# Kernel optimization log

Hardware: AMD Instinct MI355X
Metric: run time of the kernel (lower is better)

## Reference

```python
import jax, jax.numpy as jnp
import numpy as np

N = 50000      # nodes
E = 800000     # edges (before self-loops)
IN = 64        # in_channels
HID = 128      # hidden
HEADS = 4
C = HID // HEADS  # per-head dim = 32
EPS_BN = 1e-5


def setup_inputs() -> dict:
    key = jax.random.key(0)
    ks = jax.random.split(key, 40)
    f32 = jnp.float32
    def rn(i, shape, s=0.05):
        return jax.random.normal(ks[i], shape, f32) * s
    def un(i, shape, lo=0.5, hi=1.5):
        return jax.random.uniform(ks[i], shape, f32, lo, hi)
    inp = {
        'x': jax.random.normal(ks[0], (N, IN), f32),
        'edge_index': jax.random.randint(ks[1], (2, E), 0, N, jnp.int64),
        # pre: Linear(IN, HID) + BatchNorm1d(HID)
        'W_pre': rn(2, (IN, HID)), 'b_pre': rn(3, (HID,)),
        'g_pre': un(4, (HID,)), 'be_pre': rn(5, (HID,)),
        'm_pre': rn(6, (HID,), 0.1), 'v_pre': un(7, (HID,)),
        # gat1 (GATv2Conv): lin_l, lin_r, att, bias
        'Wl1': rn(8, (HID, HID)), 'bl1': rn(9, (HID,)),
        'Wr1': rn(10, (HID, HID)), 'br1': rn(11, (HID,)),
        'att1': rn(12, (HEADS, C)), 'bias1': rn(13, (HID,)),
        'g1': un(14, (HID,)), 'be1': rn(15, (HID,)),
        'm1': rn(16, (HID,), 0.1), 'v1': un(17, (HID,)),
        # gat2
        'Wl2': rn(18, (HID, HID)), 'bl2': rn(19, (HID,)),
        'Wr2': rn(20, (HID, HID)), 'br2': rn(21, (HID,)),
        'att2': rn(22, (HEADS, C)), 'bias2': rn(23, (HID,)),
        'g2': un(24, (HID,)), 'be2': rn(25, (HID,)),
        'm2': rn(26, (HID,), 0.1), 'v2': un(27, (HID,)),
        # out head: Linear(HID, HID//2) -> LeakyReLU -> Linear(HID//2, 1)
        'Wo1': rn(28, (HID, HID // 2)), 'bo1': rn(29, (HID // 2,)),
        'Wo2': rn(30, (HID // 2, 1)), 'bo2': rn(31, (1,)),
    }
    return inp


def _bn(x, g, b, m, v):
    # eval-mode BatchNorm1d with running stats
    return (x - m) * jax.lax.rsqrt(v + EPS_BN) * g + b


def _gatv2(x, src, dst, Wl, bl, Wr, br, att, bias):
    # PyG GATv2Conv, concat=True, negative_slope=0.2, eval (no dropout)
    n = x.shape[0]
    xl = (x @ Wl + bl).reshape(n, HEADS, C)   # messages from source
    xr = (x @ Wr + br).reshape(n, HEADS, C)   # target side
    xj = xl[src]                              # [E2, H, C] gather
    s = jax.nn.leaky_relu(xr[dst] + xj, 0.2)
    logits = jnp.einsum('ehc,hc->eh', s, att)  # [E2, H]
    # segment softmax over destination nodes
    mx = jax.ops.segment_max(logits, dst, num_segments=n)
    e = jnp.exp(logits - mx[dst])
    den = jax.ops.segment_sum(e, dst, num_segments=n)
    alpha = e / (den[dst] + 1e-16)
    out = jax.ops.segment_sum(xj * alpha[:, :, None], dst, num_segments=n)
    return out.reshape(n, HID) + bias


def reference(x, edge_index,
              W_pre, b_pre, g_pre, be_pre, m_pre, v_pre,
              Wl1, bl1, Wr1, br1, att1, bias1, g1, be1, m1, v1,
              Wl2, bl2, Wr2, br2, att2, bias2, g2, be2, m2, v2,
              Wo1, bo1, Wo2, bo2):
    n = x.shape[0]
    # add self loops (PyG GATv2Conv default add_self_loops=True)
    loop = jnp.arange(n, dtype=edge_index.dtype)
    src = jnp.concatenate([edge_index[0], loop])
    dst = jnp.concatenate([edge_index[1], loop])

    x = jax.nn.leaky_relu(_bn(x @ W_pre + b_pre, g_pre, be_pre, m_pre, v_pre), 0.1)
    h = x
    x = _gatv2(x, src, dst, Wl1, bl1, Wr1, br1, att1, bias1)
    x = jax.nn.leaky_relu(_bn(x, g1, be1, m1, v1), 0.1) + h
    h = x
    x = _gatv2(x, src, dst, Wl2, bl2, Wr2, br2, att2, bias2)
    x = jax.nn.leaky_relu(_bn(x, g2, be2, m2, v2), 0.1) + h
    x = jax.nn.leaky_relu(x @ Wo1 + bo1, 0.1)
    return x @ Wo2 + bo2
```

## Files before the change

kernel.cpp:

```cpp
#include <hip/hip_runtime.h>
#include <hip/hip_bf16.h>
#include <hip/hip_fp16.h>

#define NN 50000
#define EE 800000
#define SCAN_B 196

typedef unsigned int uint;
typedef unsigned short ushort;
typedef __attribute__((ext_vector_type(8))) short s16x8;
typedef __attribute__((ext_vector_type(4))) float f32x4;
typedef __attribute__((ext_vector_type(2))) _Float16 h16x2;

__device__ __forceinline__ float lrelu(float x, float s){ return fmaxf(x, x * s); }

__device__ __forceinline__ ushort bf16_rne(float x){
  uint u = __float_as_uint(x);
  return (ushort)((u + 0x7FFFu + ((u >> 16) & 1u)) >> 16);
}
__device__ __forceinline__ float bf16f(ushort h){ return __uint_as_float(((uint)h) << 16); }

__device__ __forceinline__ float dpp_add4(float x){
  int v = __float_as_int(x), t;
  t = __builtin_amdgcn_update_dpp(0, v, 0xB1, 0xF, 0xF, true);
  v = __float_as_int(__int_as_float(v) + __int_as_float(t));
  t = __builtin_amdgcn_update_dpp(0, v, 0x4E, 0xF, 0xF, true);
  v = __float_as_int(__int_as_float(v) + __int_as_float(t));
  return __int_as_float(v);
}

__device__ __forceinline__ float dpp_add16(float x){
  int v = __float_as_int(x), t;
  t = __builtin_amdgcn_update_dpp(0, v, 0xB1, 0xF, 0xF, true);
  v = __float_as_int(__int_as_float(v) + __int_as_float(t));
  t = __builtin_amdgcn_update_dpp(0, v, 0x4E, 0xF, 0xF, true);
  v = __float_as_int(__int_as_float(v) + __int_as_float(t));
  t = __builtin_amdgcn_update_dpp(0, v, 0x141, 0xF, 0xF, true);
  v = __float_as_int(__int_as_float(v) + __int_as_float(t));
  t = __builtin_amdgcn_update_dpp(0, v, 0x140, 0xF, 0xF, true);
  v = __float_as_int(__int_as_float(v) + __int_as_float(t));
  return __int_as_float(v);
}


__global__ void detect_kernel(const int* __restrict__ ei, int* __restrict__ flag){
  __shared__ int any;
  if (threadIdx.x == 0) any = 0;
  __syncthreads();
  if (ei[2 * threadIdx.x + 1] != 0) atomicOr(&any, 1);
  __syncthreads();
  if (threadIdx.x == 0) *flag = (any == 0) ? 1 : 0;
}

__global__ void zero1_kernel(int* __restrict__ a, int n){
  int i = blockIdx.x * blockDim.x + threadIdx.x;
  if (i < n) a[i] = 0;
}

__global__ void count_kernel(const int* __restrict__ ei, const int* __restrict__ flag,
                             int* __restrict__ deg){
  int e = blockIdx.x * blockDim.x + threadIdx.x;
  if (e >= EE) return;
  int d;
  if (*flag){
    const long long* eil = (const long long*)ei;
    d = (int)eil[EE + e];
  } else {
    d = ei[EE + e];
  }
  atomicAdd(&deg[d], 1);
}

__global__ void scan1_kernel(const int* __restrict__ deg, int* __restrict__ rowptr,
                             int* __restrict__ bsum){
  __shared__ int tmp[256];
  int tid = threadIdx.x;
  int idx = blockIdx.x * 256 + tid;
  int v = (idx < NN) ? deg[idx] : 0;
  tmp[tid] = v;
  __syncthreads();
  for (int off = 1; off < 256; off <<= 1){
    int t = (tid >= off) ? tmp[tid - off] : 0;
    __syncthreads();
    tmp[tid] += t;
    __syncthreads();
  }
  if (idx < NN) rowptr[idx] = tmp[tid] - v;
  if (tid == 255) bsum[blockIdx.x] = tmp[255];
}

__global__ void scan2_kernel(const int* __restrict__ bsum, int* __restrict__ boff,
                             int* __restrict__ rowptr){
  __shared__ int tmp[256];
  int tid = threadIdx.x;
  int v = (tid < SCAN_B) ? bsum[tid] : 0;
  tmp[tid] = v;
  __syncthreads();
  for (int off = 1; off < 256; off <<= 1){
    int t = (tid >= off) ? tmp[tid - off] : 0;
    __syncthreads();
    tmp[tid] += t;
    __syncthreads();
  }
  if (tid < SCAN_B) boff[tid] = tmp[tid] - v;
  if (tid == 255) rowptr[NN] = tmp[255];
}

__global__ void scan3_kernel(int* __restrict__ rowptr, const int* __restrict__ boff,
                             int* __restrict__ deg){
  int i = blockIdx.x * 256 + threadIdx.x;
  if (i < NN){ rowptr[i] += boff[blockIdx.x]; deg[i] = 0; }
}

__global__ void scatter_kernel(const int* __restrict__ ei, const int* __restrict__ flag,
                               const int* __restrict__ rowptr, int* __restrict__ cursor,
                               int* __restrict__ csr_src){
  int e = blockIdx.x * blockDim.x + threadIdx.x;
  if (e >= EE) return;
  int s, d;
  if (*flag){
    const long long* eil = (const long long*)ei;
    s = (int)eil[e];
    d = (int)eil[EE + e];
  } else {
    s = ei[e];
    d = ei[EE + e];
  }
  int pos = atomicAdd(&cursor[d], 1);
  csr_src[rowptr[d] + pos] = s;
}

__global__ void prep_w_kernel(const float* __restrict__ w0, const float* __restrict__ w1,
                              const float* __restrict__ w2, const float* __restrict__ w3,
                              const float* __restrict__ w4, const float* __restrict__ w5,
                              ushort* __restrict__ wt){
  int gid = blockIdx.x * 256 + threadIdx.x;
  if (gid >= 81920) return;
  const int KK[6]    = {64, 128, 128, 128, 128, 128};
  const int CC[6]    = {128, 128, 128, 128, 128, 64};
  const int cumel[7] = {0, 8192, 24576, 40960, 57344, 73728, 81920};
  int j = 0;
  while (gid >= cumel[j + 1]) j++;
  int local = gid - cumel[j];
  int K = KK[j], C = CC[j];
  int k = local / C, c = local % C;
  const float* src = (j == 0) ? w0 : (j == 1) ? w1 : (j == 2) ? w2 : (j == 3) ? w3 : (j == 4) ? w4 : w5;
  wt[cumel[j] + c * K + k] = bf16_rne(src[local]);
}

template<int KIN, int NOUT, int EPI, bool DUAL, bool FUSE>
__launch_bounds__(256, 2)
__global__ void mfma_gemm_kernel(const float* __restrict__ A,
                                 const ushort* __restrict__ Wt, const float* __restrict__ bias,
                                 const ushort* __restrict__ Wt2, const float* __restrict__ bias2,
                                 const float* __restrict__ bn_g, const float* __restrict__ bn_b,
                                 const float* __restrict__ bn_m, const float* __restrict__ bn_v,
                                 ushort* __restrict__ OUTH, float* __restrict__ OUTF, int n){
  constexpr int KF = KIN / 32;
  constexpr int NF = NOUT / 16;
  constexpr int WELEM = KIN * NOUT;
  constexpr int NW = DUAL ? 2 : 1;
  __shared__ ushort sW[NW * WELEM];
  const int tid  = threadIdx.x;
  const int wave = tid >> 6, lane = tid & 63;
  const int fr = lane & 15;
  const int kg = lane >> 4;
  const int r0 = blockIdx.x * 128 + wave * 32;

  for (int i = tid; i < NW * WELEM / 8; i += 256){
    const ushort* src = (i * 8 < WELEM) ? (Wt + i * 8) : (Wt2 + (i * 8 - WELEM));
    uint4 w = *reinterpret_cast<const uint4*>(src);
    uint b = (uint)i * 16u;
    uint sb = b ^ (((b >> 8) & 7u) << 4);
    *reinterpret_cast<uint4*>((char*)sW + sb) = w;
  }

  const int ar0 = min(r0 + fr,      n - 1);
  const int ar1 = min(r0 + 16 + fr, n - 1);

  s16x8 ah[2][KF], al[2][KF];
  #pragma unroll
  for (int kf = 0; kf < KF; kf++){
    const float* p0 = A + (size_t)ar0 * KIN + kf * 32 + kg * 8;
    const float* p1 = A + (size_t)ar1 * KIN + kf * 32 + kg * 8;
    float4 a0 = *reinterpret_cast<const float4*>(p0);
    float4 b0 = *reinterpret_cast<const float4*>(p0 + 4);
    float4 a1 = *reinterpret_cast<const float4*>(p1);
    float4 b1 = *reinterpret_cast<const float4*>(p1 + 4);
    float f0[8] = {a0.x, a0.y, a0.z, a0.w, b0.x, b0.y, b0.z, b0.w};
    float f1[8] = {a1.x, a1.y, a1.z, a1.w, b1.x, b1.y, b1.z, b1.w};
    #pragma unroll
    for (int j = 0; j < 8; j++){
      ushort h0 = bf16_rne(f0[j]);
      ah[0][kf][j] = (short)h0;
      al[0][kf][j] = (short)bf16_rne(f0[j] - bf16f(h0));
      ushort h1 = bf16_rne(f1[j]);
      ah[1][kf][j] = (short)h1;
      al[1][kf][j] = (short)bf16_rne(f1[j] - bf16f(h1));
    }
  }
  __syncthreads();

  f32x4 acc[2][NF];

#define GEMM_PHASE(PH)                                                                    \
  {                                                                                       \
    _Pragma("unroll")                                                                     \
    for (int nf = 0; nf < NF; nf++){                                                      \
      s16x8 wh[KF];                                                                       \
      _Pragma("unroll")                                                                   \
      for (int kf = 0; kf < KF; kf++){                                                    \
        uint b = (uint)(((PH) * WELEM + (nf * 16 + fr) * KIN + kf * 32 + kg * 8) * 2);    \
        wh[kf] = *reinterpret_cast<const s16x8*>((const char*)sW + (b ^ (((b >> 8) & 7u) << 4))); \
      }                                                                                   \
      _Pragma("unroll")                                                                   \
      for (int kf = 0; kf < KF; kf++){                                                    \
        acc[0][nf] = __builtin_amdgcn_mfma_f32_16x16x32_bf16(ah[0][kf], wh[kf], acc[0][nf], 0, 0, 0); \
        acc[1][nf] = __builtin_amdgcn_mfma_f32_16x16x32_bf16(ah[1][kf], wh[kf], acc[1][nf], 0, 0, 0); \
        acc[0][nf] = __builtin_amdgcn_mfma_f32_16x16x32_bf16(al[0][kf], wh[kf], acc[0][nf], 0, 0, 0); \
        acc[1][nf] = __builtin_amdgcn_mfma_f32_16x16x32_bf16(al[1][kf], wh[kf], acc[1][nf], 0, 0, 0); \
      }                                                                                   \
    }                                                                                     \
  }

  #pragma unroll
  for (int nf = 0; nf < NF; nf++){ acc[0][nf] = (f32x4){0.f,0.f,0.f,0.f}; acc[1][nf] = (f32x4){0.f,0.f,0.f,0.f}; }
  GEMM_PHASE(0)

  float rowdot[2][4];
  if (FUSE){
    #pragma unroll
    for (int rg = 0; rg < 2; rg++)
      #pragma unroll
      for (int i = 0; i < 4; i++) rowdot[rg][i] = 0.f;
  }

  #pragma unroll
  for (int nf = 0; nf < NF; nf++){
    int c = nf * 16 + fr;
    float bb = bias[c];
    float w2 = FUSE ? bias2[c] : 0.f;
    float g_ = 0.f, b_ = 0.f, m_ = 0.f, v_ = 0.f;
    if (EPI == 1){ g_ = bn_g[c]; b_ = bn_b[c]; m_ = bn_m[c]; v_ = bn_v[c]; }
    #pragma unroll
    for (int rg = 0; rg < 2; rg++){
      #pragma unroll
      for (int i = 0; i < 4; i++){
        int gr = r0 + rg * 16 + kg * 4 + i;
        if (gr < n){
          float v = acc[rg][nf][i] + bb;
          if (EPI == 1){
            v = (v - m_) * rsqrtf(v_ + 1e-5f) * g_ + b_;
            v = lrelu(v, 0.1f);
          }
          if (EPI == 2){ v = lrelu(v, 0.1f); }
          if (FUSE){
            rowdot[rg][i] = fmaf(v, w2, rowdot[rg][i]);
          } else if (DUAL){
            __half hv = __float2half(v);
            OUTH[(size_t)gr * NOUT + c] = *reinterpret_cast<ushort*>(&hv);
          } else {
            OUTF[(size_t)gr * NOUT + c] = v;
          }
        }
      }
    }
  }

  if (FUSE){
    float bo2 = bn_g[0];
    #pragma unroll
    for (int rg = 0; rg < 2; rg++){
      #pragma unroll
      for (int i = 0; i < 4; i++){
        float rd = dpp_add16(rowdot[rg][i]);
        int gr = r0 + rg * 16 + kg * 4 + i;
        if (fr == 0 && gr < n) OUTF[gr] = rd + bo2;
      }
    }
  }

  if (DUAL){
    #pragma unroll
    for (int nf = 0; nf < NF; nf++){ acc[0][nf] = (f32x4){0.f,0.f,0.f,0.f}; acc[1][nf] = (f32x4){0.f,0.f,0.f,0.f}; }
    GEMM_PHASE(1)
    #pragma unroll
    for (int nf = 0; nf < NF; nf++){
      int c = nf * 16 + fr;
      float bb = bias2[c];
      #pragma unroll
      for (int rg = 0; rg < 2; rg++){
        #pragma unroll
        for (int i = 0; i < 4; i++){
          int gr = r0 + rg * 16 + kg * 4 + i;
          if (gr < n) OUTF[(size_t)gr * NOUT + c] = acc[rg][nf][i] + bb;
        }
      }
    }
  }
#undef GEMM_PHASE
}

__global__ void gat_edge_kernel(const uint* __restrict__ XLh, const float* __restrict__ XR,
                                const float* __restrict__ att, const float* __restrict__ bias,
                                const float* __restrict__ bn_g, const float* __restrict__ bn_b,
                                const float* __restrict__ bn_m, const float* __restrict__ bn_v,
                                const float* __restrict__ H, float* __restrict__ OUT,
                                const int* __restrict__ rowptr, const int* __restrict__ csr_src,
                                int n){
  const int wid  = (int)((blockIdx.x * blockDim.x + threadIdx.x) >> 6);
  const int lane = threadIdx.x & 63;
  const int nb = wid * 4;
  if (nb >= n) return;
  const int g  = lane >> 4;
  const int c4 = lane & 15;
  const int cb = c4 * 8;
  const int d  = min(nb + g, n - 1);
  const float L2E = 1.44269504f;

  float4 xr0 = *reinterpret_cast<const float4*>(XR + (size_t)d * 128 + cb);
  float4 xr1 = *reinterpret_cast<const float4*>(XR + (size_t)d * 128 + cb + 4);
  float4 at0 = *reinterpret_cast<const float4*>(att + cb);
  float4 at1 = *reinterpret_cast<const float4*>(att + cb + 4);
  __half2 xrh[4] = { __floats2half2_rn(xr0.x, xr0.y), __floats2half2_rn(xr0.z, xr0.w),
                     __floats2half2_rn(xr1.x, xr1.y), __floats2half2_rn(xr1.z, xr1.w) };
  __half2 ath[4] = { __floats2half2_rn(at0.x * L2E, at0.y * L2E), __floats2half2_rn(at0.z * L2E, at0.w * L2E),
                     __floats2half2_rn(at1.x * L2E, at1.y * L2E), __floats2half2_rn(at1.z * L2E, at1.w * L2E) };
  const __half2 c06 = __float2half2_rn(0.6f);
  const __half2 c04 = __float2half2_rn(0.4f);

  float den = 0.f;
  float O[8] = {0.f,0.f,0.f,0.f,0.f,0.f,0.f,0.f};

  const int start = rowptr[d];
  const int cnt = rowptr[d + 1] - start + 1;
  const int* __restrict__ base = csr_src + start - 1;

  int mx = cnt;
  mx = max(mx, __shfl_xor(mx, 16));
  mx = max(mx, __shfl_xor(mx, 32));

  auto IDX = [&](int s) -> int {
    int c = min(s, cnt - 1);
    return (c == 0) ? d : base[c];
  };
  auto ROW = [&](int si) -> uint4 {
    return *reinterpret_cast<const uint4*>(XLh + (size_t)si * 64 + c4 * 4);
  };

  auto PROC = [&](uint4 cur, int s){
    const bool valid = s < cnt;
    __half2 x0 = *reinterpret_cast<__half2*>(&cur.x);
    __half2 x1 = *reinterpret_cast<__half2*>(&cur.y);
    __half2 x2 = *reinterpret_cast<__half2*>(&cur.z);
    __half2 x3 = *reinterpret_cast<__half2*>(&cur.w);
    __half2 s0 = __hadd2(xrh[0], x0);
    __half2 s1 = __hadd2(xrh[1], x1);
    __half2 s2 = __hadd2(xrh[2], x2);
    __half2 s3 = __hadd2(xrh[3], x3);
    uint a0u = *reinterpret_cast<uint*>(&s0) & 0x7FFF7FFFu;
    uint a1u = *reinterpret_cast<uint*>(&s1) & 0x7FFF7FFFu;
    uint a2u = *reinterpret_cast<uint*>(&s2) & 0x7FFF7FFFu;
    uint a3u = *reinterpret_cast<uint*>(&s3) & 0x7FFF7FFFu;
    __half2 l0 = __hfma2(c06, s0, __hmul2(c04, *reinterpret_cast<__half2*>(&a0u)));
    __half2 l1 = __hfma2(c06, s1, __hmul2(c04, *reinterpret_cast<__half2*>(&a1u)));
    __half2 l2 = __hfma2(c06, s2, __hmul2(c04, *reinterpret_cast<__half2*>(&a2u)));
    __half2 l3 = __hfma2(c06, s3, __hmul2(c04, *reinterpret_cast<__half2*>(&a3u)));
#if __has_builtin(__builtin_amdgcn_fdot2)
    float acc = __builtin_amdgcn_fdot2(*reinterpret_cast<h16x2*>(&ath[0]), *reinterpret_cast<h16x2*>(&l0), 0.f, false);
    acc = __builtin_amdgcn_fdot2(*reinterpret_cast<h16x2*>(&ath[1]), *reinterpret_cast<h16x2*>(&l1), acc, false);
    acc = __builtin_amdgcn_fdot2(*reinterpret_cast<h16x2*>(&ath[2]), *reinterpret_cast<h16x2*>(&l2), acc, false);
    acc = __builtin_amdgcn_fdot2(*reinterpret_cast<h16x2*>(&ath[3]), *reinterpret_cast<h16x2*>(&l3), acc, false);
#else
    float2 q0 = __half22float2(l0), q1 = __half22float2(l1), q2 = __half22float2(l2), q3 = __half22float2(l3);
    float2 p0 = __half22float2(ath[0]), p1 = __half22float2(ath[1]), p2 = __half22float2(ath[2]), p3 = __half22float2(ath[3]);
    float acc = q0.x*p0.x + q0.y*p0.y + q1.x*p1.x + q1.y*p1.y
              + q2.x*p2.x + q2.y*p2.y + q3.x*p3.x + q3.y*p3.y;
#endif
    acc = dpp_add4(acc);
    float w = valid ? exp2f(acc) : 0.f;
    den += w;
    float2 f0 = __half22float2(x0), f1 = __half22float2(x1);
    float2 f2 = __half22float2(x2), f3 = __half22float2(x3);
    O[0] = fmaf(w, f0.x, O[0]);  O[1] = fmaf(w, f0.y, O[1]);
    O[2] = fmaf(w, f1.x, O[2]);  O[3] = fmaf(w, f1.y, O[3]);
    O[4] = fmaf(w, f2.x, O[4]);  O[5] = fmaf(w, f2.y, O[5]);
    O[6] = fmaf(w, f3.x, O[6]);  O[7] = fmaf(w, f3.y, O[7]);
  };

  uint4 r0 = ROW(IDX(0)), r1 = ROW(IDX(1)), r2 = ROW(IDX(2));
  for (int s = 0; s < mx; s++){
    int j3 = IDX(s + 3);
    PROC(r0, s);
    r0 = r1; r1 = r2; r2 = ROW(j3);
  }

  {
    float inv = 1.f / (den + 1e-16f);
    float4 bi0 = *reinterpret_cast<const float4*>(bias + cb);
    float4 bi1 = *reinterpret_cast<const float4*>(bias + cb + 4);
    float4 g0 = *reinterpret_cast<const float4*>(bn_g + cb);
    float4 g1 = *reinterpret_cast<const float4*>(bn_g + cb + 4);
    float4 bb0 = *reinterpret_cast<const float4*>(bn_b + cb);
    float4 bb1 = *reinterpret_cast<const float4*>(bn_b + cb + 4);
    float4 mm0 = *reinterpret_cast<const float4*>(bn_m + cb);
    float4 mm1 = *reinterpret_cast<const float4*>(bn_m + cb + 4);
    float4 vv0 = *reinterpret_cast<const float4*>(bn_v + cb);
    float4 vv1 = *reinterpret_cast<const float4*>(bn_v + cb + 4);
    float4 h0 = *reinterpret_cast<const float4*>(H + (size_t)d * 128 + cb);
    float4 h1 = *reinterpret_cast<const float4*>(H + (size_t)d * 128 + cb + 4);
    float bi[8] = {bi0.x,bi0.y,bi0.z,bi0.w,bi1.x,bi1.y,bi1.z,bi1.w};
    float gg[8] = {g0.x,g0.y,g0.z,g0.w,g1.x,g1.y,g1.z,g1.w};
    float bbv[8]= {bb0.x,bb0.y,bb0.z,bb0.w,bb1.x,bb1.y,bb1.z,bb1.w};
    float mmv[8]= {mm0.x,mm0.y,mm0.z,mm0.w,mm1.x,mm1.y,mm1.z,mm1.w};
    float vvv[8]= {vv0.x,vv0.y,vv0.z,vv0.w,vv1.x,vv1.y,vv1.z,vv1.w};
    float hh[8] = {h0.x,h0.y,h0.z,h0.w,h1.x,h1.y,h1.z,h1.w};
    float r[8];
    #pragma unroll
    for (int j = 0; j < 8; j++){
      float v = O[j] * inv + bi[j];
      v = (v - mmv[j]) * rsqrtf(vvv[j] + 1e-5f) * gg[j] + bbv[j];
      r[j] = lrelu(v, 0.1f) + hh[j];
    }
    *reinterpret_cast<float4*>(OUT + (size_t)d * 128 + cb)     = make_float4(r[0], r[1], r[2], r[3]);
    *reinterpret_cast<float4*>(OUT + (size_t)d * 128 + cb + 4) = make_float4(r[4], r[5], r[6], r[7]);
  }
}

extern "C" void kernel_launch(void* const* d_in, const int* in_sizes, int n_in,
                              void* d_out, int out_size, void* d_ws, size_t ws_size,
                              hipStream_t stream) {
  const float* x     = (const float*)d_in[0];
  const int*   ei    = (const int*)  d_in[1];
  const float* W_pre = (const float*)d_in[2];
  const float* b_pre = (const float*)d_in[3];
  const float* g_pre = (const float*)d_in[4];
  const float* be_pre= (const float*)d_in[5];
  const float* m_pre = (const float*)d_in[6];
  const float* v_pre = (const float*)d_in[7];
  const float* Wl1  = (const float*)d_in[8];
  const float* bl1  = (const float*)d_in[9];
  const float* Wr1  = (const float*)d_in[10];
  const float* br1  = (const float*)d_in[11];
  const float* att1 = (const float*)d_in[12];
  const float* bias1= (const float*)d_in[13];
  const float* g1   = (const float*)d_in[14];
  const float* be1  = (const float*)d_in[15];
  const float* m1   = (const float*)d_in[16];
  const float* v1   = (const float*)d_in[17];
  const float* Wl2  = (const float*)d_in[18];
  const float* bl2  = (const float*)d_in[19];
  const float* Wr2  = (const float*)d_in[20];
  const float* br2  = (const float*)d_in[21];
  const float* att2 = (const float*)d_in[22];
  const float* bias2= (const float*)d_in[23];
  const float* g2   = (const float*)d_in[24];
  const float* be2  = (const float*)d_in[25];
  const float* m2   = (const float*)d_in[26];
  const float* v2   = (const float*)d_in[27];
  const float* Wo1  = (const float*)d_in[28];
  const float* bo1  = (const float*)d_in[29];
  const float* Wo2  = (const float*)d_in[30];
  const float* bo2  = (const float*)d_in[31];
  float* out = (float*)d_out;
  char*  ws  = (char*)d_ws;

  float*  buf0 = (float*)(ws + 0);
  float*  buf2 = (float*)(ws + 25600000);
  uint*   hbuf = (uint*) (ws + 51200000);
  int* rowptr = (int*)(ws + 64000000);
  int* deg    = (int*)(ws + 64200448);
  int* bsum   = (int*)(ws + 64400448);
  int* boff   = (int*)(ws + 64401472);
  int* csr    = (int*)(ws + 64600448);
  int* flag   = (int*)(ws + 67800448);
  ushort* wt  = (ushort*)(ws + 68000000);

  const ushort* wtPre = wt;
  const ushort* wtL1  = wt + 8192;
  const ushort* wtR1  = wt + 24576;
  const ushort* wtL2  = wt + 40960;
  const ushort* wtR2  = wt + 57344;
  const ushort* wtO1  = wt + 73728;

  detect_kernel<<<1, 256, 0, stream>>>(ei, flag);
  zero1_kernel<<<SCAN_B, 256, 0, stream>>>(deg, NN);
  count_kernel<<<(EE + 255) / 256, 256, 0, stream>>>(ei, flag, deg);
  scan1_kernel<<<SCAN_B, 256, 0, stream>>>(deg, rowptr, bsum);
  scan2_kernel<<<1, 256, 0, stream>>>(bsum, boff, rowptr);
  scan3_kernel<<<SCAN_B, 256, 0, stream>>>(rowptr, boff, deg);
  scatter_kernel<<<(EE + 255) / 256, 256, 0, stream>>>(ei, flag, rowptr, deg, csr);

  prep_w_kernel<<<320, 256, 0, stream>>>(W_pre, Wl1, Wr1, Wl2, Wr2, Wo1, wt);

  const int GB = (NN + 127) / 128;
  const int GW = (NN + 15) / 16;

  mfma_gemm_kernel<64, 128, 1, false, false><<<GB, 256, 0, stream>>>(
      x, wtPre, b_pre, nullptr, nullptr,
      g_pre, be_pre, m_pre, v_pre, nullptr, buf0, NN);
  mfma_gemm_kernel<128, 128, 0, true, false><<<GB, 256, 0, stream>>>(
      buf0, wtL1, bl1, wtR1, br1,
      nullptr, nullptr, nullptr, nullptr, (ushort*)hbuf, buf2, NN);
  gat_edge_kernel<<<GW, 256, 0, stream>>>(hbuf, buf2, att1, bias1, g1, be1, m1, v1,
                                          buf0 , buf2 , rowptr, csr, NN);
  mfma_gemm_kernel<128, 128, 0, true, false><<<GB, 256, 0, stream>>>(
      buf2, wtL2, bl2, wtR2, br2,
      nullptr, nullptr, nullptr, nullptr, (ushort*)hbuf, buf0, NN);
  gat_edge_kernel<<<GW, 256, 0, stream>>>(hbuf, buf0, att2, bias2, g2, be2, m2, v2,
                                          buf2 , buf0 , rowptr, csr, NN);
  mfma_gemm_kernel<128, 64, 2, false, true><<<GB, 256, 0, stream>>>(
      buf0, wtO1, bo1, nullptr, Wo2,
      bo2, nullptr, nullptr, nullptr, nullptr, out, NN);
}
```

Before: 272.3 us.

## Merge CSR build kernels into weight prep and GEMM launches as extra blocks

```diff
diff --git a/kernel.cpp b/kernel.cpp
--- a/kernel.cpp
+++ b/kernel.cpp
@@ -5,6 +5,7 @@
 #define NN 50000
 #define EE 800000
 #define SCAN_B 196
+#define EB 3125
 
 typedef unsigned int uint;
 typedef unsigned short ushort;
@@ -42,33 +43,37 @@
   return __int_as_float(v);
 }
 
-
-__global__ void detect_kernel(const int* __restrict__ ei, int* __restrict__ flag){
-  __shared__ int any;
-  if (threadIdx.x == 0) any = 0;
-  __syncthreads();
-  if (ei[2 * threadIdx.x + 1] != 0) atomicOr(&any, 1);
-  __syncthreads();
-  if (threadIdx.x == 0) *flag = (any == 0) ? 1 : 0;
-}
-
-__global__ void zero1_kernel(int* __restrict__ a, int n){
-  int i = blockIdx.x * blockDim.x + threadIdx.x;
-  if (i < n) a[i] = 0;
-}
-
-__global__ void count_kernel(const int* __restrict__ ei, const int* __restrict__ flag,
-                             int* __restrict__ deg){
-  int e = blockIdx.x * blockDim.x + threadIdx.x;
-  if (e >= EE) return;
-  int d;
-  if (*flag){
-    const long long* eil = (const long long*)ei;
-    d = (int)eil[EE + e];
+__global__ void prep_misc_kernel(const float* __restrict__ w0, const float* __restrict__ w1,
+                                 const float* __restrict__ w2, const float* __restrict__ w3,
+                                 const float* __restrict__ w4, const float* __restrict__ w5,
+                                 ushort* __restrict__ wt,
+                                 const int* __restrict__ ei, int* __restrict__ flag,
+                                 int* __restrict__ deg){
+  const int b = blockIdx.x;
+  if (b < 320){
+    int gid = b * 256 + threadIdx.x;
+    if (gid >= 81920) return;
+    const int KK[6]    = {64, 128, 128, 128, 128, 128};
+    const int CC[6]    = {128, 128, 128, 128, 128, 64};
+    const int cumel[7] = {0, 8192, 24576, 40960, 57344, 73728, 81920};
+    int j = 0;
+    while (gid >= cumel[j + 1]) j++;
+    int local = gid - cumel[j];
+    int K = KK[j], C = CC[j];
+    int k = local / C, c = local % C;
+    const float* src = (j == 0) ? w0 : (j == 1) ? w1 : (j == 2) ? w2 : (j == 3) ? w3 : (j == 4) ? w4 : w5;
+    wt[cumel[j] + c * K + k] = bf16_rne(src[local]);
+  } else if (b < 320 + SCAN_B){
+    int i = (b - 320) * 256 + threadIdx.x;
+    if (i < NN) deg[i] = 0;
   } else {
-    d = ei[EE + e];
-  }
-  atomicAdd(&deg[d], 1);
+    __shared__ int any;
+    if (threadIdx.x == 0) any = 0;
+    __syncthreads();
+    if (ei[2 * threadIdx.x + 1] != 0) atomicOr(&any, 1);
+    __syncthreads();
+    if (threadIdx.x == 0) *flag = (any == 0) ? 1 : 0;
+  }
 }
 
 __global__ void scan1_kernel(const int* __restrict__ deg, int* __restrict__ rowptr,
@@ -112,10 +117,23 @@
   if (i < NN){ rowptr[i] += boff[blockIdx.x]; deg[i] = 0; }
 }
 
-__global__ void scatter_kernel(const int* __restrict__ ei, const int* __restrict__ flag,
-                               const int* __restrict__ rowptr, int* __restrict__ cursor,
-                               int* __restrict__ csr_src){
-  int e = blockIdx.x * blockDim.x + threadIdx.x;
+__device__ __forceinline__ void count_body(int e, const int* __restrict__ ei,
+                                           const int* __restrict__ flag, int* __restrict__ deg){
+  if (e >= EE) return;
+  int d;
+  if (*flag){
+    const long long* eil = (const long long*)ei;
+    d = (int)eil[EE + e];
+  } else {
+    d = ei[EE + e];
+  }
+  atomicAdd(&deg[d], 1);
+}
+
+__device__ __forceinline__ void scatter_body(int e, const int* __restrict__ ei,
+                                             const int* __restrict__ flag,
+                                             const int* __restrict__ rowptr,
+                                             int* __restrict__ cursor, int* __restrict__ csr){
   if (e >= EE) return;
   int s, d;
   if (*flag){
@@ -127,30 +145,12 @@
     d = ei[EE + e];
   }
   int pos = atomicAdd(&cursor[d], 1);
-  csr_src[rowptr[d] + pos] = s;
-}
-
-__global__ void prep_w_kernel(const float* __restrict__ w0, const float* __restrict__ w1,
-                              const float* __restrict__ w2, const float* __restrict__ w3,
-                              const float* __restrict__ w4, const float* __restrict__ w5,
-                              ushort* __restrict__ wt){
-  int gid = blockIdx.x * 256 + threadIdx.x;
-  if (gid >= 81920) return;
-  const int KK[6]    = {64, 128, 128, 128, 128, 128};
-  const int CC[6]    = {128, 128, 128, 128, 128, 64};
-  const int cumel[7] = {0, 8192, 24576, 40960, 57344, 73728, 81920};
-  int j = 0;
-  while (gid >= cumel[j + 1]) j++;
-  int local = gid - cumel[j];
-  int K = KK[j], C = CC[j];
-  int k = local / C, c = local % C;
-  const float* src = (j == 0) ? w0 : (j == 1) ? w1 : (j == 2) ? w2 : (j == 3) ? w3 : (j == 4) ? w4 : w5;
-  wt[cumel[j] + c * K + k] = bf16_rne(src[local]);
+  csr[rowptr[d] + pos] = s;
 }
 
 template<int KIN, int NOUT, int EPI, bool DUAL, bool FUSE>
-__launch_bounds__(256, 2)
-__global__ void mfma_gemm_kernel(const float* __restrict__ A,
+__device__ __forceinline__ void gemm_body(int bid,
+                                 const float* __restrict__ A,
                                  const ushort* __restrict__ Wt, const float* __restrict__ bias,
                                  const ushort* __restrict__ Wt2, const float* __restrict__ bias2,
                                  const float* __restrict__ bn_g, const float* __restrict__ bn_b,
@@ -165,7 +165,7 @@
   const int wave = tid >> 6, lane = tid & 63;
   const int fr = lane & 15;
   const int kg = lane >> 4;
-  const int r0 = blockIdx.x * 128 + wave * 32;
+  const int r0 = bid * 128 + wave * 32;
 
   for (int i = tid; i < NW * WELEM / 8; i += 256){
     const ushort* src = (i * 8 < WELEM) ? (Wt + i * 8) : (Wt2 + (i * 8 - WELEM));
@@ -299,6 +299,29 @@
     }
   }
 #undef GEMM_PHASE
+}
+
+template<int KIN, int NOUT, int EPI, bool DUAL, bool FUSE, int TAIL>
+__launch_bounds__(256, 2)
+__global__ void mfma_gemm_kernel(const float* __restrict__ A,
+                                 const ushort* __restrict__ Wt, const float* __restrict__ bias,
+                                 const ushort* __restrict__ Wt2, const float* __restrict__ bias2,
+                                 const float* __restrict__ bn_g, const float* __restrict__ bn_b,
+                                 const float* __restrict__ bn_m, const float* __restrict__ bn_v,
+                                 ushort* __restrict__ OUTH, float* __restrict__ OUTF, int n,
+                                 int gemmBlocks,
+                                 const int* __restrict__ ei, const int* __restrict__ flag,
+                                 int* __restrict__ deg, const int* __restrict__ rowptr,
+                                 int* __restrict__ csr){
+  if ((int)blockIdx.x < gemmBlocks){
+    gemm_body<KIN, NOUT, EPI, DUAL, FUSE>(blockIdx.x, A, Wt, bias, Wt2, bias2,
+                                          bn_g, bn_b, bn_m, bn_v, OUTH, OUTF, n);
+    return;
+  }
+  if (TAIL == 0) return;
+  int e = ((int)blockIdx.x - gemmBlocks) * 256 + (int)threadIdx.x;
+  if (TAIL == 1) count_body(e, ei, flag, deg);
+  if (TAIL == 2) scatter_body(e, ei, flag, rowptr, deg, csr);
 }
 
 __global__ void gat_edge_kernel(const uint* __restrict__ XLh, const float* __restrict__ XR,
@@ -483,33 +506,39 @@
   const ushort* wtR2  = wt + 57344;
   const ushort* wtO1  = wt + 73728;
 
-  detect_kernel<<<1, 256, 0, stream>>>(ei, flag);
-  zero1_kernel<<<SCAN_B, 256, 0, stream>>>(deg, NN);
-  count_kernel<<<(EE + 255) / 256, 256, 0, stream>>>(ei, flag, deg);
+  const int GB = (NN + 127) / 128;
+  const int GW = (NN + 15) / 16;
+
+  prep_misc_kernel<<<320 + SCAN_B + 1, 256, 0, stream>>>(
+      W_pre, Wl1, Wr1, Wl2, Wr2, Wo1, wt, ei, flag, deg);
+
+  mfma_gemm_kernel<64, 128, 1, false, false, 1><<<GB + EB, 256, 0, stream>>>(
+      x, wtPre, b_pre, nullptr, nullptr,
+      g_pre, be_pre, m_pre, v_pre, nullptr, buf0, NN,
+      GB, ei, flag, deg, nullptr, nullptr);
+
   scan1_kernel<<<SCAN_B, 256, 0, stream>>>(deg, rowptr, bsum);
   scan2_kernel<<<1, 256, 0, stream>>>(bsum, boff, rowptr);
   scan3_kernel<<<SCAN_B, 256, 0, stream>>>(rowptr, boff, deg);
-  scatter_kernel<<<(EE + 255) / 256, 256, 0, stream>>>(ei, flag, rowptr, deg, csr);
-
-  prep_w_kernel<<<320, 256, 0, stream>>>(W_pre, Wl1, Wr1, Wl2, Wr2, Wo1, wt);
-
-  const int GB = (NN + 127) / 128;
-  const int GW = (NN + 15) / 16;
-
-  mfma_gemm_kernel<64, 128, 1, false, false><<<GB, 256, 0, stream>>>(
-      x, wtPre, b_pre, nullptr, nullptr,
-      g_pre, be_pre, m_pre, v_pre, nullptr, buf0, NN);
-  mfma_gemm_kernel<128, 128, 0, true, false><<<GB, 256, 0, stream>>>(
+
+  mfma_gemm_kernel<128, 128, 0, true, false, 2><<<GB + EB, 256, 0, stream>>>(
       buf0, wtL1, bl1, wtR1, br1,
-      nullptr, nullptr, nullptr, nullptr, (ushort*)hbuf, buf2, NN);
+      nullptr, nullptr, nullptr, nullptr, (ushort*)hbuf, buf2, NN,
+      GB, ei, flag, deg, rowptr, csr);
+
   gat_edge_kernel<<<GW, 256, 0, stream>>>(hbuf, buf2, att1, bias1, g1, be1, m1, v1,
                                           buf0 , buf2 , rowptr, csr, NN);
-  mfma_gemm_kernel<128, 128, 0, true, false><<<GB, 256, 0, stream>>>(
+
+  mfma_gemm_kernel<128, 128, 0, true, false, 0><<<GB, 256, 0, stream>>>(
       buf2, wtL2, bl2, wtR2, br2,
-      nullptr, nullptr, nullptr, nullptr, (ushort*)hbuf, buf0, NN);
+      nullptr, nullptr, nullptr, nullptr, (ushort*)hbuf, buf0, NN,
+      GB, nullptr, nullptr, nullptr, nullptr, nullptr);
+
   gat_edge_kernel<<<GW, 256, 0, stream>>>(hbuf, buf0, att2, bias2, g2, be2, m2, v2,
                                           buf2 , buf0 , rowptr, csr, NN);
-  mfma_gemm_kernel<128, 64, 2, false, true><<<GB, 256, 0, stream>>>(
+
+  mfma_gemm_kernel<128, 64, 2, false, true, 0><<<GB, 256, 0, stream>>>(
       buf0, wtO1, bo1, nullptr, Wo2,
-      bo2, nullptr, nullptr, nullptr, nullptr, out, NN);
-}
+      bo2, nullptr, nullptr, nullptr, nullptr, out, NN,
+      GB, nullptr, nullptr, nullptr, nullptr, nullptr);
+}
```

New measurement: 247.2 us. 1.1x faster.
